# Kernel optimization log

Measured on AMD Instinct MI355X. Metric: run time of the kernel, lower is better.

## Reference

```python
import jax, jax.numpy as jnp
import numpy as np

B, S, D_IN, D_MID, D_OUT, V = 32, 512, 768, 128, 4, 100000
N = B * S  # static upper bound on number of unique (vocab_id, batch_id) pairs


def setup_inputs() -> dict:
    key = jax.random.key(0)
    k1, k2, k3, k4 = jax.random.split(key, 4)
    vocab_ids = jax.random.randint(k1, (B, S), 0, V)
    embeddings = jax.random.normal(k2, (B, S, D_IN), jnp.float32)
    # nn.Linear default init (kaiming-uniform-ish); exact distribution is irrelevant for correctness
    lin_bound = 1.0 / np.sqrt(D_IN)
    W1 = jax.random.uniform(k3, (D_IN, D_MID), jnp.float32, -lin_bound, lin_bound)
    b1 = jnp.zeros((D_MID,), jnp.float32)
    # kaiming_uniform_(a=sqrt(5)) on (V, D_MID, D_OUT): fan_in = D_MID*D_OUT, bound = 1/sqrt(fan_in)
    enc_bound = 1.0 / np.sqrt(D_MID * D_OUT)
    encoder_weights = jax.random.uniform(k4, (V, D_MID, D_OUT), jnp.float32, -enc_bound, enc_bound)
    return {"vocab_ids": vocab_ids, "embeddings": embeddings, "W1": W1, "b1": b1,
            "encoder_weights": encoder_weights}


def reference(vocab_ids, embeddings, W1, b1, encoder_weights):
    # Composite key = vocab_id * B + batch_id -> same lexicographic (vocab, batch) order
    # as torch.unique(dim=0) on stacked (vocab_id, batch_id) pairs.
    batch_ids = jnp.arange(B, dtype=vocab_ids.dtype)[:, None]            # (B,1)
    keys = (vocab_ids * B + batch_ids).reshape(-1)                        # (N,)
    # Static-size unique for jit; padded slots (fill) receive zero-sum embeddings.
    uniq_keys, inv = jnp.unique(keys, size=N, fill_value=0, return_inverse=True)
    flat_emb = embeddings.reshape(N, D_IN)
    summed = jax.ops.segment_sum(flat_emb, inv.reshape(-1), num_segments=N)  # (N, D_IN)
    h = jnp.tanh(summed @ W1 + b1)                                        # (N, D_MID)
    uniq_vocab = uniq_keys // B
    uniq_batch = uniq_keys % B
    Wtok = encoder_weights[uniq_vocab]                                    # (N, D_MID, D_OUT) gather
    encoded = jax.nn.sigmoid(jnp.einsum('bi,bio->bo', h, Wtok))           # (N, D_OUT)
    ids = jnp.stack([uniq_vocab, uniq_batch], axis=1)                     # (N, 2)
    return ids, encoded
```

## Files before the change

kernel.cpp:

```cpp
#include <hip/hip_runtime.h>
#include <hip/hip_bf16.h>

#define NELEM 16384
#define DIN 768
#define DMID 128
#define DOUT 4

typedef __attribute__((ext_vector_type(8))) short short8;
typedef __attribute__((ext_vector_type(4))) float f32x4;

__device__ __forceinline__ unsigned f2bf(float f) {
    unsigned u = __float_as_uint(f);
    return (u + 0x7FFFu + ((u >> 16) & 1u)) >> 16;
}
__device__ __forceinline__ unsigned wscan_inc(unsigned x, int lane) {
    unsigned inc = x;
#pragma unroll
    for (int off = 1; off < 64; off <<= 1) {
        unsigned y = __shfl_up(inc, off);
        if (lane >= off) inc += y;
    }
    return inc;
}

#define FAST6_WS 983168

__global__ __launch_bounds__(256) void prep_kernel(
    const int* __restrict__ vocab_ids, const float* __restrict__ W1,
    unsigned* __restrict__ Gb, unsigned short* __restrict__ WtG,
    unsigned* __restrict__ RB, unsigned long long* __restrict__ stage,
    unsigned* __restrict__ LCnt) {
    const int t = threadIdx.x;
    const int blk = blockIdx.x;

    if (blk >= 32) {
        int o = (blk - 32) * 1024 + t * 4;
        int c = o / DIN;
        int k = o - c * DIN;
        unsigned p0 = f2bf(W1[(k + 0) * DMID + c]) | (f2bf(W1[(k + 1) * DMID + c]) << 16);
        unsigned p1 = f2bf(W1[(k + 2) * DMID + c]) | (f2bf(W1[(k + 3) * DMID + c]) << 16);
        uint2 pk2; pk2.x = p0; pk2.y = p1;
        *(uint2*)(WtG + (size_t)c * DIN + k) = pk2;
        return;
    }

    __shared__ unsigned lbm[4096];
    __shared__ unsigned voc[512];
    __shared__ unsigned short gel[512];
    __shared__ unsigned gcnt[512];
    __shared__ unsigned gstart[512];
    __shared__ unsigned part[256];
    __shared__ unsigned wsumL[4];

    const int b = blk;
    const int lane = t & 63;
    const int wv = t >> 6;

#pragma unroll
    for (int i = 0; i < 16; ++i) lbm[t + 256 * i] = 0;
    gcnt[t] = 0; gcnt[t + 256] = 0;
#pragma unroll
    for (int q = 0; q < 2; ++q) {
        int s = q * 256 + t;
        voc[s] = (unsigned)vocab_ids[b * 512 + s];
    }
    __syncthreads();
#pragma unroll
    for (int q = 0; q < 2; ++q) {
        unsigned v = voc[q * 256 + t];
        atomicOr(&lbm[v >> 5], 1u << (v & 31u));
    }
    __syncthreads();
#pragma unroll
    for (int i = 0; i < 4; ++i) {
        int w4 = i * 256 + t;
        uint4 x;
        x.x = lbm[w4 * 4 + 0]; x.y = lbm[w4 * 4 + 1];
        x.z = lbm[w4 * 4 + 2]; x.w = lbm[w4 * 4 + 3];
        *(uint4*)(RB + (size_t)b * 4096 + w4 * 4) = x;
    }
    {
        unsigned sum = 0;
#pragma unroll
        for (int j = 0; j < 16; ++j) sum += (unsigned)__popc(lbm[t * 16 + j]);
        unsigned inc = wscan_inc(sum, lane);
        if (lane == 63) wsumL[wv] = inc;
        __syncthreads();
        unsigned woff = 0;
        for (int i = 0; i < wv; ++i) woff += wsumL[i];
        part[t] = woff + inc - sum;
        if (t == 255) LCnt[b] = woff + inc;
        __syncthreads();
    }
#pragma unroll
    for (int q = 0; q < 2; ++q) {
        int s = q * 256 + t;
        unsigned v = voc[s];
        unsigned lw = v >> 5, c = lw >> 4;
        unsigned g = part[c];
        for (unsigned j = c * 16; j < lw; ++j) g += (unsigned)__popc(lbm[j]);
        g += (unsigned)__popc(lbm[lw] & ((1u << (v & 31u)) - 1u));
        gel[s] = (unsigned short)g;
        atomicAdd(&gcnt[g], 1u);
    }
    __syncthreads();
    {
        unsigned a = gcnt[2 * t], b2 = gcnt[2 * t + 1];
        unsigned pair = a + b2;
        unsigned inc = wscan_inc(pair, lane);
        if (lane == 63) wsumL[wv] = inc;
        __syncthreads();
        unsigned woff = 0;
        for (int i = 0; i < wv; ++i) woff += wsumL[i];
        unsigned excl = woff + inc - pair;
        gstart[2 * t] = excl;
        gstart[2 * t + 1] = excl + a;
    }
    __syncthreads();
#pragma unroll
    for (int q = 0; q < 2; ++q) {
        int s = q * 256 + t;
        unsigned g = gel[s];
        unsigned v = voc[s];
        unsigned m = 0;
        if (gcnt[g] > 1) {
            for (int j = 0; j < s; ++j) if (voc[j] == v) ++m;
        }
        Gb[b * 512 + gstart[g] + m] = (v << 9) | (unsigned)s;
        if (m == 0) {
            unsigned sdval = ((unsigned)b << 19) | (gstart[g] << 10) | gcnt[g];
            stage[b * 512 + g] = ((unsigned long long)v << 32) | sdval;
        }
    }
}

__global__ __launch_bounds__(256) void rank_kernel(
    const unsigned* __restrict__ RB,
    const unsigned long long* __restrict__ stage,
    const unsigned* __restrict__ LCnt,
    unsigned* __restrict__ SD, float* __restrict__ out_ids) {
    __shared__ unsigned pre1[4096];
    __shared__ unsigned wsumL[4];
    __shared__ unsigned Ush;

    const int t = threadIdx.x;
    const int b = blockIdx.x;
    const int lane = t & 63;
    const int wv = t >> 6;
    const uint4* rb4 = (const uint4*)RB;

    {
        unsigned cs[16];
#pragma unroll
        for (int i = 0; i < 16; ++i) cs[i] = 0;
#pragma unroll 4
        for (int b2 = 0; b2 < 32; ++b2) {
            const uint4* rp = rb4 + b2 * 1024 + t * 4;
#pragma unroll
            for (int q = 0; q < 4; ++q) {
                uint4 x = rp[q];
                cs[q * 4 + 0] += (unsigned)__popc(x.x);
                cs[q * 4 + 1] += (unsigned)__popc(x.y);
                cs[q * 4 + 2] += (unsigned)__popc(x.z);
                cs[q * 4 + 3] += (unsigned)__popc(x.w);
            }
        }
        unsigned loc[16];
        unsigned run = 0;
#pragma unroll
        for (int i = 0; i < 16; ++i) { loc[i] = run; run += cs[i]; }
        unsigned inc = wscan_inc(run, lane);
        if (lane == 63) wsumL[wv] = inc;
        __syncthreads();
        unsigned woff = 0;
        for (int i = 0; i < wv; ++i) woff += wsumL[i];
        unsigned excl = woff + inc - run;
#pragma unroll
        for (int i = 0; i < 16; ++i) pre1[t * 16 + i] = excl + loc[i];
        if (t == 255) Ush = woff + inc;
        __syncthreads();
    }
    const unsigned U = Ush;

    const unsigned cnt = LCnt[b];
    for (unsigned l = t; l < cnt; l += 256) {
        unsigned long long sv = stage[b * 512 + l];
        unsigned v = (unsigned)(sv >> 32);
        unsigned sdval = (unsigned)sv;
        unsigned w = v >> 5, bit = v & 31u;
        unsigned maskLT = (1u << bit) - 1u;
        unsigned rank = pre1[w];
#pragma unroll 8
        for (int b2 = 0; b2 < 32; ++b2) {
            unsigned word = RB[b2 * 4096 + w];
            rank += (unsigned)__popc(word & maskLT);
            if (b2 < b) rank += (word >> bit) & 1u;
        }
        SD[rank] = sdval;
        out_ids[2 * rank + 0] = (float)v;
        out_ids[2 * rank + 1] = (float)b;
    }
    for (int u = (int)U + b * 256 + t; u < NELEM; u += 32 * 256) {
        SD[u] = 0u;
        out_ids[2 * u + 0] = 0.0f;
        out_ids[2 * u + 1] = 0.0f;
    }
}

#define FBM 16
__global__ __launch_bounds__(256) void fused_kernel(
    const unsigned* __restrict__ Gb,
    const unsigned* __restrict__ SD,
    const unsigned short* __restrict__ WtG,
    const float* __restrict__ emb,
    const float* __restrict__ b1,
    const float* __restrict__ enc,
    float* __restrict__ out_enc) {
    __shared__ char smem[20736];

    const int t = threadIdx.x;
    const int u0 = blockIdx.x * FBM;
    const int l = t & 63;
    const int w = t >> 6;

    const int ar = t >> 4;
    const int ak4 = t & 15;
    const unsigned sdw = SD[u0 + ar];
    const int lenA = (int)(sdw & 1023u);
    const unsigned embBase = (sdw >> 19) << 9;
    const unsigned gb0 = embBase + ((sdw >> 10) & 511u);

    f32x4 acc0 = {0.f, 0.f, 0.f, 0.f};
    f32x4 acc1 = {0.f, 0.f, 0.f, 0.f};

    for (int kk = 0; kk < DIN; kk += 64) {
        __syncthreads();
        {
            float s0 = 0.f, s1 = 0.f, s2 = 0.f, s3 = 0.f;
            const float* base = emb + (size_t)(kk + ak4 * 4);
            for (int p = 0; p < lenA; ++p) {
                unsigned idx = embBase + (Gb[gb0 + p] & 511u);
                const float4 e4 = *(const float4*)(base + (size_t)idx * DIN);
                s0 += e4.x; s1 += e4.y; s2 += e4.z; s3 += e4.w;
            }
            uint2 packed;
            packed.x = f2bf(s0) | (f2bf(s1) << 16);
            packed.y = f2bf(s2) | (f2bf(s3) << 16);
            *(uint2*)(smem + ar * 144 + ak4 * 8) = packed;
        }
        {
#pragma unroll
            for (int i = 0; i < 4; ++i) {
                int q = t + i * 256;
                int c = q >> 3;
                int uo = q & 7;
                uint4 dv = *(const uint4*)(WtG + (size_t)c * DIN + kk + uo * 8);
                *(uint4*)(smem + 2304 + c * 144 + uo * 16) = dv;
            }
        }
        __syncthreads();
        {
            const int arow = l & 15;
            const int ull = l >> 4;
#pragma unroll
            for (int kf = 0; kf < 2; ++kf) {
                short8 aF = *(const short8*)(smem + arow * 144 + kf * 64 + ull * 16);
                short8 bF0 = *(const short8*)(smem + 2304 + (w * 32 + arow) * 144 + kf * 64 + ull * 16);
                short8 bF1 = *(const short8*)(smem + 2304 + (w * 32 + 16 + arow) * 144 + kf * 64 + ull * 16);
                acc0 = __builtin_amdgcn_mfma_f32_16x16x32_bf16(aF, bF0, acc0, 0, 0, 0);
                acc1 = __builtin_amdgcn_mfma_f32_16x16x32_bf16(aF, bF1, acc1, 0, 0, 0);
            }
        }
    }
    __syncthreads();
    {
        float* Hs = (float*)smem;
        const int col0 = w * 32 + (l & 15);
        const int rbase = (l >> 4) * 4;
#pragma unroll
        for (int reg = 0; reg < 4; ++reg) {
            Hs[(rbase + reg) * 132 + col0] = tanhf(acc0[reg] + b1[col0]);
            Hs[(rbase + reg) * 132 + col0 + 16] = tanhf(acc1[reg] + b1[col0 + 16]);
        }
    }
    __syncthreads();
    {
        const float* Hs = (const float*)smem;
        const int r = t >> 4;
        const int g = t & 15;
        const int u = u0 + r;
        const unsigned sdw2 = SD[u];
        unsigned vocab = 0;
        if (sdw2 & 1023u)
            vocab = Gb[((sdw2 >> 19) << 9) + ((sdw2 >> 10) & 511u)] >> 9;
        const float4* wrow = (const float4*)(enc + (size_t)vocab * (DMID * DOUT));
        float ax = 0.f, ay = 0.f, az = 0.f, aw = 0.f;
#pragma unroll
        for (int jj = 0; jj < 8; ++jj) {
            int j = jj * 16 + g;
            float4 w4 = wrow[j];
            float hv = Hs[r * 132 + j];
            ax += hv * w4.x; ay += hv * w4.y; az += hv * w4.z; aw += hv * w4.w;
        }
#pragma unroll
        for (int off = 1; off < 16; off <<= 1) {
            ax += __shfl_xor(ax, off);
            ay += __shfl_xor(ay, off);
            az += __shfl_xor(az, off);
            aw += __shfl_xor(aw, off);
        }
        if (g == 0) {
            float4 o;
            o.x = 1.f / (1.f + expf(-ax));
            o.y = 1.f / (1.f + expf(-ay));
            o.z = 1.f / (1.f + expf(-az));
            o.w = 1.f / (1.f + expf(-aw));
            *(float4*)(out_enc + (size_t)u * 4) = o;
        }
    }
}

#define SORT_SMEM (65536 + 65536 + 4096 + 64)

__global__ __launch_bounds__(1024) void sort_transpose_kernel(
    const int* __restrict__ vocab_ids,
    const float* __restrict__ W1,
    unsigned int* __restrict__ G,
    unsigned short* __restrict__ RS,
    unsigned short* __restrict__ WtG,
    float* __restrict__ out_ids) {
    const int t = threadIdx.x;
    if (blockIdx.x != 0) {
        int idx = (blockIdx.x - 1) * 1024 + t;
        if (idx < DMID * DIN) {
            int c = idx / DIN;
            int k = idx - c * DIN;
            WtG[idx] = (unsigned short)f2bf(W1[k * DMID + c]);
        }
        return;
    }
    extern __shared__ char smem[];
    unsigned* Gs     = (unsigned*)smem;
    unsigned* histDM = (unsigned*)(smem + 65536);
    unsigned* sums   = (unsigned*)(smem + 131072);
    unsigned* totalU = (unsigned*)(smem + 135168);
    for (int e = t; e < NELEM; e += 1024)
        Gs[e] = ((unsigned)vocab_ids[e] << 14) | (unsigned)e;
    __syncthreads();
    for (int pass = 0; pass < 6; ++pass) {
        const int shift = 9 + pass * 4;
        unsigned v[16];
#pragma unroll
        for (int i = 0; i < 16; ++i) v[i] = Gs[t * 16 + i];
#pragma unroll
        for (int d = 0; d < 16; ++d) histDM[d * 1024 + t] = 0;
#pragma unroll
        for (int i = 0; i < 16; ++i) histDM[((v[i] >> shift) & 15u) * 1024 + t] += 1;
        __syncthreads();
        unsigned lex[16]; unsigned run = 0;
#pragma unroll
        for (int i = 0; i < 16; ++i) { unsigned x = histDM[t * 16 + i]; lex[i] = run; run += x; }
        sums[t] = run;
        __syncthreads();
        if (t < 64) {
            unsigned s[16]; unsigned tot = 0;
#pragma unroll
            for (int i = 0; i < 16; ++i) { unsigned x = sums[t * 16 + i]; s[i] = tot; tot += x; }
            unsigned incv = tot;
#pragma unroll
            for (int off = 1; off < 64; off <<= 1) {
                unsigned y = __shfl_up(incv, off);
                if (t >= off) incv += y;
            }
            unsigned excl = incv - tot;
#pragma unroll
            for (int i = 0; i < 16; ++i) sums[t * 16 + i] = excl + s[i];
        }
        __syncthreads();
#pragma unroll
        for (int i = 0; i < 16; ++i) histDM[t * 16 + i] = sums[t] + lex[i];
        __syncthreads();
        unsigned mycnt[16];
#pragma unroll
        for (int d = 0; d < 16; ++d) mycnt[d] = histDM[d * 1024 + t];
#pragma unroll
        for (int i = 0; i < 16; ++i) {
            unsigned d = (v[i] >> shift) & 15u;
            Gs[mycnt[d]++] = v[i];
        }
        __syncthreads();
    }
    unsigned v[16];
#pragma unroll
    for (int i = 0; i < 16; ++i) v[i] = Gs[t * 16 + i];
    unsigned pk = (t == 0) ? 0xFFFFFFFFu : (Gs[t * 16 - 1] >> 9);
    unsigned fm = 0;
#pragma unroll
    for (int i = 0; i < 16; ++i) {
        unsigned key = v[i] >> 9;
        if (key != pk) fm |= (1u << i);
        pk = key;
    }
    sums[t] = (unsigned)__popc(fm);
    __syncthreads();
    if (t < 64) {
        unsigned s[16]; unsigned tot = 0;
#pragma unroll
        for (int i = 0; i < 16; ++i) { unsigned x = sums[t * 16 + i]; s[i] = tot; tot += x; }
        unsigned incv = tot;
#pragma unroll
        for (int off = 1; off < 64; off <<= 1) {
            unsigned y = __shfl_up(incv, off);
            if (t >= off) incv += y;
        }
        unsigned excl = incv - tot;
#pragma unroll
        for (int i = 0; i < 16; ++i) sums[t * 16 + i] = excl + s[i];
        if (t == 63) *totalU = incv;
    }
    __syncthreads();
    unsigned r = sums[t];
#pragma unroll
    for (int i = 0; i < 16; ++i) {
        if (fm & (1u << i)) {
            RS[r] = (unsigned short)(t * 16 + i);
            out_ids[2 * r + 0] = (float)(v[i] >> 14);
            out_ids[2 * r + 1] = (float)((v[i] >> 9) & 31u);
            ++r;
        }
    }
    const unsigned U = *totalU;
    for (int u = t; u < NELEM; u += 1024) {
        if ((unsigned)u >= U) {
            RS[u] = (unsigned short)NELEM;
            out_ids[2 * u + 0] = 0.0f;
            out_ids[2 * u + 1] = 0.0f;
        }
        G[u] = Gs[u];
    }
    if (t == 0) RS[NELEM] = (unsigned short)NELEM;
}

__global__ __launch_bounds__(256) void fused_kernel_rs(
    const unsigned* __restrict__ G,
    const unsigned short* __restrict__ RS,
    const unsigned short* __restrict__ WtG,
    const float* __restrict__ emb,
    const float* __restrict__ b1,
    const float* __restrict__ enc,
    float* __restrict__ out_enc) {
    __shared__ char smem[20736];
    const int t = threadIdx.x;
    const int u0 = blockIdx.x * FBM;
    const int l = t & 63;
    const int w = t >> 6;
    const int ar = t >> 4;
    const int ak4 = t & 15;
    const int rs_a = (int)RS[u0 + ar];
    const int re_a = (int)RS[u0 + ar + 1];
    f32x4 acc0 = {0.f, 0.f, 0.f, 0.f};
    f32x4 acc1 = {0.f, 0.f, 0.f, 0.f};
    for (int kk = 0; kk < DIN; kk += 64) {
        __syncthreads();
        {
            float s0 = 0.f, s1 = 0.f, s2 = 0.f, s3 = 0.f;
            const float* base = emb + (size_t)(kk + ak4 * 4);
            for (int p = rs_a; p < re_a; ++p) {
                unsigned idx = G[p] & 16383u;
                const float4 e4 = *(const float4*)(base + (size_t)idx * DIN);
                s0 += e4.x; s1 += e4.y; s2 += e4.z; s3 += e4.w;
            }
            uint2 packed;
            packed.x = f2bf(s0) | (f2bf(s1) << 16);
            packed.y = f2bf(s2) | (f2bf(s3) << 16);
            *(uint2*)(smem + ar * 144 + ak4 * 8) = packed;
        }
        {
#pragma unroll
            for (int i = 0; i < 4; ++i) {
                int q = t + i * 256;
                int c = q >> 3;
                int uo = q & 7;
                uint4 dv = *(const uint4*)(WtG + (size_t)c * DIN + kk + uo * 8);
                *(uint4*)(smem + 2304 + c * 144 + uo * 16) = dv;
            }
        }
        __syncthreads();
        {
            const int arow = l & 15;
            const int ull = l >> 4;
#pragma unroll
            for (int kf = 0; kf < 2; ++kf) {
                short8 aF = *(const short8*)(smem + arow * 144 + kf * 64 + ull * 16);
                short8 bF0 = *(const short8*)(smem + 2304 + (w * 32 + arow) * 144 + kf * 64 + ull * 16);
                short8 bF1 = *(const short8*)(smem + 2304 + (w * 32 + 16 + arow) * 144 + kf * 64 + ull * 16);
                acc0 = __builtin_amdgcn_mfma_f32_16x16x32_bf16(aF, bF0, acc0, 0, 0, 0);
                acc1 = __builtin_amdgcn_mfma_f32_16x16x32_bf16(aF, bF1, acc1, 0, 0, 0);
            }
        }
    }
    __syncthreads();
    {
        float* Hs = (float*)smem;
        const int col0 = w * 32 + (l & 15);
        const int rbase = (l >> 4) * 4;
#pragma unroll
        for (int reg = 0; reg < 4; ++reg) {
            Hs[(rbase + reg) * 132 + col0] = tanhf(acc0[reg] + b1[col0]);
            Hs[(rbase + reg) * 132 + col0 + 16] = tanhf(acc1[reg] + b1[col0 + 16]);
        }
    }
    __syncthreads();
    {
        const float* Hs = (const float*)smem;
        const int r = t >> 4;
        const int g = t & 15;
        const int u = u0 + r;
        const int rs = (int)RS[u];
        const int re = (int)RS[u + 1];
        unsigned vocab = (rs < re) ? (G[rs] >> 14) : 0u;
        const float4* wrow = (const float4*)(enc + (size_t)vocab * (DMID * DOUT));
        float ax = 0.f, ay = 0.f, az = 0.f, aw = 0.f;
#pragma unroll
        for (int jj = 0; jj < 8; ++jj) {
            int j = jj * 16 + g;
            float4 w4 = wrow[j];
            float hv = Hs[r * 132 + j];
            ax += hv * w4.x; ay += hv * w4.y; az += hv * w4.z; aw += hv * w4.w;
        }
#pragma unroll
        for (int off = 1; off < 16; off <<= 1) {
            ax += __shfl_xor(ax, off);
            ay += __shfl_xor(ay, off);
            az += __shfl_xor(az, off);
            aw += __shfl_xor(aw, off);
        }
        if (g == 0) {
            float4 o;
            o.x = 1.f / (1.f + expf(-ax));
            o.y = 1.f / (1.f + expf(-ay));
            o.z = 1.f / (1.f + expf(-az));
            o.w = 1.f / (1.f + expf(-aw));
            *(float4*)(out_enc + (size_t)u * 4) = o;
        }
    }
}

extern "C" void kernel_launch(void* const* d_in, const int* in_sizes, int n_in,
                              void* d_out, int out_size, void* d_ws, size_t ws_size,
                              hipStream_t stream) {
    const int*   vocab_ids = (const int*)d_in[0];
    const float* emb       = (const float*)d_in[1];
    const float* W1        = (const float*)d_in[2];
    const float* b1        = (const float*)d_in[3];
    const float* enc       = (const float*)d_in[4];
    float* out = (float*)d_out;
    float* out_ids = out;
    float* out_enc = out + NELEM * 2;
    char* ws = (char*)d_ws;

    if (ws_size >= FAST6_WS) {
        unsigned*           Gb    = (unsigned*)(ws + 0);
        unsigned*           SD    = (unsigned*)(ws + 65536);
        unsigned short*     WtG   = (unsigned short*)(ws + 131072);
        unsigned long long* stage = (unsigned long long*)(ws + 327680);
        unsigned*           LCnt  = (unsigned*)(ws + 458752);
        unsigned*           RB    = (unsigned*)(ws + 458880);

        prep_kernel<<<128, 256, 0, stream>>>(vocab_ids, W1, Gb, WtG, RB, stage, LCnt);
        rank_kernel<<<32, 256, 0, stream>>>(RB, stage, LCnt, SD, out_ids);
        fused_kernel<<<NELEM / FBM, 256, 0, stream>>>(Gb, SD, WtG, emb, b1, enc, out_enc);
    } else {
        unsigned int*   G   = (unsigned int*)(ws);
        unsigned short* RS  = (unsigned short*)(ws + 65536);
        unsigned short* WtG = (unsigned short*)(ws + 98432);

        hipFuncSetAttribute((const void*)sort_transpose_kernel,
                            hipFuncAttributeMaxDynamicSharedMemorySize, SORT_SMEM);
        sort_transpose_kernel<<<1 + 96, 1024, SORT_SMEM, stream>>>(
            vocab_ids, W1, G, RS, WtG, out_ids);
        fused_kernel_rs<<<NELEM / FBM, 256, 0, stream>>>(G, RS, WtG, emb, b1, enc, out_enc);
    }
}
```

Before: 60.08 us.

## Merge prep and rank kernels into one launch with grid-wide atomic barriers

Combines the bitmap/group-building prep kernel and the rank kernel into a single 64-block kernel that uses atomic-counter grid barriers instead of a kernel boundary. The bf16 transpose of W1 is spread over 32 blocks instead of 96. The column popcount reduction over the 32 batch bitmaps is spread across all 64 blocks and stored in a small CS buffer, so the rank phase reads precomputed counts instead of each block re-reading the full bitmap set. Adds nontemporal stores and a memset for the barrier counter, and relies on all 64 blocks being co-resident.

```diff
diff --git a/kernel.cpp b/kernel.cpp
--- a/kernel.cpp
+++ b/kernel.cpp
@@ -8,6 +8,8 @@
 
 typedef __attribute__((ext_vector_type(8))) short short8;
 typedef __attribute__((ext_vector_type(4))) float f32x4;
+typedef __attribute__((ext_vector_type(2))) unsigned uint32x2;
+typedef __attribute__((ext_vector_type(4))) unsigned uint32x4;
 
 __device__ __forceinline__ unsigned f2bf(float f) {
     unsigned u = __float_as_uint(f);
@@ -23,147 +25,165 @@
     return inc;
 }
 
-#define FAST6_WS 983168
-
-__global__ __launch_bounds__(256) void prep_kernel(
+__device__ __forceinline__ void gbar(unsigned* cnt, unsigned thresh) {
+    __syncthreads();
+    if (threadIdx.x == 0) {
+        __hip_atomic_fetch_add(cnt, 1u, __ATOMIC_ACQ_REL, __HIP_MEMORY_SCOPE_AGENT);
+        while (__hip_atomic_load(cnt, __ATOMIC_RELAXED, __HIP_MEMORY_SCOPE_AGENT) < thresh)
+            __builtin_amdgcn_s_sleep(1);
+        (void)__hip_atomic_load(cnt, __ATOMIC_ACQUIRE, __HIP_MEMORY_SCOPE_AGENT);
+    }
+    __syncthreads();
+}
+
+#define FAST7_WS 999616
+
+__global__ __launch_bounds__(256) void merged_kernel(
     const int* __restrict__ vocab_ids, const float* __restrict__ W1,
-    unsigned* __restrict__ Gb, unsigned short* __restrict__ WtG,
-    unsigned* __restrict__ RB, unsigned long long* __restrict__ stage,
-    unsigned* __restrict__ LCnt) {
-    const int t = threadIdx.x;
-    const int blk = blockIdx.x;
-
-    if (blk >= 32) {
-        int o = (blk - 32) * 1024 + t * 4;
-        int c = o / DIN;
-        int k = o - c * DIN;
-        unsigned p0 = f2bf(W1[(k + 0) * DMID + c]) | (f2bf(W1[(k + 1) * DMID + c]) << 16);
-        unsigned p1 = f2bf(W1[(k + 2) * DMID + c]) | (f2bf(W1[(k + 3) * DMID + c]) << 16);
-        uint2 pk2; pk2.x = p0; pk2.y = p1;
-        *(uint2*)(WtG + (size_t)c * DIN + k) = pk2;
-        return;
-    }
-
+    unsigned* __restrict__ Gb, unsigned* __restrict__ SD,
+    unsigned short* __restrict__ WtG,
+    unsigned long long* __restrict__ stage, unsigned* __restrict__ LCnt,
+    unsigned* __restrict__ RB, unsigned* __restrict__ CS,
+    unsigned* __restrict__ bar, float* __restrict__ out_ids) {
     __shared__ unsigned lbm[4096];
     __shared__ unsigned voc[512];
     __shared__ unsigned short gel[512];
     __shared__ unsigned gcnt[512];
     __shared__ unsigned gstart[512];
     __shared__ unsigned part[256];
+    __shared__ unsigned colred[256];
     __shared__ unsigned wsumL[4];
-
-    const int b = blk;
+    __shared__ unsigned Ush;
+
+    const int t = threadIdx.x;
+    const int blk = blockIdx.x;
     const int lane = t & 63;
     const int wv = t >> 6;
 
-#pragma unroll
-    for (int i = 0; i < 16; ++i) lbm[t + 256 * i] = 0;
-    gcnt[t] = 0; gcnt[t + 256] = 0;
-#pragma unroll
-    for (int q = 0; q < 2; ++q) {
-        int s = q * 256 + t;
-        voc[s] = (unsigned)vocab_ids[b * 512 + s];
-    }
-    __syncthreads();
-#pragma unroll
-    for (int q = 0; q < 2; ++q) {
-        unsigned v = voc[q * 256 + t];
-        atomicOr(&lbm[v >> 5], 1u << (v & 31u));
-    }
-    __syncthreads();
-#pragma unroll
-    for (int i = 0; i < 4; ++i) {
-        int w4 = i * 256 + t;
-        uint4 x;
-        x.x = lbm[w4 * 4 + 0]; x.y = lbm[w4 * 4 + 1];
-        x.z = lbm[w4 * 4 + 2]; x.w = lbm[w4 * 4 + 3];
-        *(uint4*)(RB + (size_t)b * 4096 + w4 * 4) = x;
-    }
+    if (blk >= 32) {
+        int base = (blk - 32) * 256 + t;
+        int c = base >> 6;
+        int k0 = (base & 63) * 12;
+#pragma unroll
+        for (int j = 0; j < 3; ++j) {
+            int k = k0 + j * 4;
+            uint32x2 pk2;
+            pk2.x = f2bf(W1[(k + 0) * DMID + c]) | (f2bf(W1[(k + 1) * DMID + c]) << 16);
+            pk2.y = f2bf(W1[(k + 2) * DMID + c]) | (f2bf(W1[(k + 3) * DMID + c]) << 16);
+            __builtin_nontemporal_store(pk2, (uint32x2*)(WtG + (size_t)c * DIN + k));
+        }
+    } else {
+        const int b = blk;
+#pragma unroll
+        for (int i = 0; i < 16; ++i) lbm[t + 256 * i] = 0;
+        gcnt[t] = 0; gcnt[t + 256] = 0;
+#pragma unroll
+        for (int q = 0; q < 2; ++q) {
+            int s = q * 256 + t;
+            voc[s] = (unsigned)vocab_ids[b * 512 + s];
+        }
+        __syncthreads();
+#pragma unroll
+        for (int q = 0; q < 2; ++q) {
+            unsigned v = voc[q * 256 + t];
+            atomicOr(&lbm[v >> 5], 1u << (v & 31u));
+        }
+        __syncthreads();
+#pragma unroll
+        for (int i = 0; i < 4; ++i) {
+            int w4 = i * 256 + t;
+            uint32x4 x;
+            x.x = lbm[w4 * 4 + 0]; x.y = lbm[w4 * 4 + 1];
+            x.z = lbm[w4 * 4 + 2]; x.w = lbm[w4 * 4 + 3];
+            __builtin_nontemporal_store(x, (uint32x4*)(RB + (size_t)b * 4096 + w4 * 4));
+        }
+        {
+            unsigned sum = 0;
+#pragma unroll
+            for (int j = 0; j < 16; ++j) sum += (unsigned)__popc(lbm[t * 16 + j]);
+            unsigned inc = wscan_inc(sum, lane);
+            if (lane == 63) wsumL[wv] = inc;
+            __syncthreads();
+            unsigned woff = 0;
+            for (int i = 0; i < wv; ++i) woff += wsumL[i];
+            part[t] = woff + inc - sum;
+            if (t == 255) __builtin_nontemporal_store(woff + inc, LCnt + b);
+            __syncthreads();
+        }
+#pragma unroll
+        for (int q = 0; q < 2; ++q) {
+            int s = q * 256 + t;
+            unsigned v = voc[s];
+            unsigned lw = v >> 5, c = lw >> 4;
+            unsigned g = part[c];
+            for (unsigned j = c * 16; j < lw; ++j) g += (unsigned)__popc(lbm[j]);
+            g += (unsigned)__popc(lbm[lw] & ((1u << (v & 31u)) - 1u));
+            gel[s] = (unsigned short)g;
+            atomicAdd(&gcnt[g], 1u);
+        }
+        __syncthreads();
+        {
+            unsigned a = gcnt[2 * t], b2 = gcnt[2 * t + 1];
+            unsigned pair = a + b2;
+            unsigned inc = wscan_inc(pair, lane);
+            if (lane == 63) wsumL[wv] = inc;
+            __syncthreads();
+            unsigned woff = 0;
+            for (int i = 0; i < wv; ++i) woff += wsumL[i];
+            unsigned excl = woff + inc - pair;
+            gstart[2 * t] = excl;
+            gstart[2 * t + 1] = excl + a;
+        }
+        __syncthreads();
+#pragma unroll
+        for (int q = 0; q < 2; ++q) {
+            int s = q * 256 + t;
+            unsigned g = gel[s];
+            unsigned v = voc[s];
+            unsigned m = 0;
+            if (gcnt[g] > 1) {
+                for (int j = 0; j < s; ++j) if (voc[j] == v) ++m;
+            }
+            __builtin_nontemporal_store((v << 9) | (unsigned)s,
+                                        Gb + b * 512 + gstart[g] + m);
+            if (m == 0) {
+                unsigned sdval = ((unsigned)b << 19) | (gstart[g] << 10) | gcnt[g];
+                __builtin_nontemporal_store(((unsigned long long)v << 32) | sdval,
+                                            stage + b * 512 + g);
+            }
+        }
+    }
+
+    gbar(bar, 64);
+
     {
-        unsigned sum = 0;
-#pragma unroll
-        for (int j = 0; j < 16; ++j) sum += (unsigned)__popc(lbm[t * 16 + j]);
-        unsigned inc = wscan_inc(sum, lane);
-        if (lane == 63) wsumL[wv] = inc;
-        __syncthreads();
-        unsigned woff = 0;
-        for (int i = 0; i < wv; ++i) woff += wsumL[i];
-        part[t] = woff + inc - sum;
-        if (t == 255) LCnt[b] = woff + inc;
-        __syncthreads();
-    }
-#pragma unroll
-    for (int q = 0; q < 2; ++q) {
-        int s = q * 256 + t;
-        unsigned v = voc[s];
-        unsigned lw = v >> 5, c = lw >> 4;
-        unsigned g = part[c];
-        for (unsigned j = c * 16; j < lw; ++j) g += (unsigned)__popc(lbm[j]);
-        g += (unsigned)__popc(lbm[lw] & ((1u << (v & 31u)) - 1u));
-        gel[s] = (unsigned short)g;
-        atomicAdd(&gcnt[g], 1u);
-    }
-    __syncthreads();
-    {
-        unsigned a = gcnt[2 * t], b2 = gcnt[2 * t + 1];
-        unsigned pair = a + b2;
-        unsigned inc = wscan_inc(pair, lane);
-        if (lane == 63) wsumL[wv] = inc;
-        __syncthreads();
-        unsigned woff = 0;
-        for (int i = 0; i < wv; ++i) woff += wsumL[i];
-        unsigned excl = woff + inc - pair;
-        gstart[2 * t] = excl;
-        gstart[2 * t + 1] = excl + a;
-    }
-    __syncthreads();
-#pragma unroll
-    for (int q = 0; q < 2; ++q) {
-        int s = q * 256 + t;
-        unsigned g = gel[s];
-        unsigned v = voc[s];
-        unsigned m = 0;
-        if (gcnt[g] > 1) {
-            for (int j = 0; j < s; ++j) if (voc[j] == v) ++m;
-        }
-        Gb[b * 512 + gstart[g] + m] = (v << 9) | (unsigned)s;
-        if (m == 0) {
-            unsigned sdval = ((unsigned)b << 19) | (gstart[g] << 10) | gcnt[g];
-            stage[b * 512 + g] = ((unsigned long long)v << 32) | sdval;
-        }
-    }
-}
-
-__global__ __launch_bounds__(256) void rank_kernel(
-    const unsigned* __restrict__ RB,
-    const unsigned long long* __restrict__ stage,
-    const unsigned* __restrict__ LCnt,
-    unsigned* __restrict__ SD, float* __restrict__ out_ids) {
-    __shared__ unsigned pre1[4096];
-    __shared__ unsigned wsumL[4];
-    __shared__ unsigned Ush;
-
-    const int t = threadIdx.x;
-    const int b = blockIdx.x;
-    const int lane = t & 63;
-    const int wv = t >> 6;
-    const uint4* rb4 = (const uint4*)RB;
-
+        const int w = blk * 64 + lane;
+        const int r0 = wv * 8;
+        unsigned partial = 0;
+#pragma unroll
+        for (int r = 0; r < 8; ++r)
+            partial += (unsigned)__popc(RB[(size_t)(r0 + r) * 4096 + w]);
+        colred[t] = partial;
+        __syncthreads();
+        if (t < 64) {
+            unsigned cs = colred[t] + colred[t + 64] + colred[t + 128] + colred[t + 192];
+            __builtin_nontemporal_store(cs, CS + blk * 64 + t);
+        }
+    }
+
+    gbar(bar, 128);
+
+    if (blk >= 32) return;
+
+    const int b = blk;
     {
         unsigned cs[16];
-#pragma unroll
-        for (int i = 0; i < 16; ++i) cs[i] = 0;
-#pragma unroll 4
-        for (int b2 = 0; b2 < 32; ++b2) {
-            const uint4* rp = rb4 + b2 * 1024 + t * 4;
-#pragma unroll
-            for (int q = 0; q < 4; ++q) {
-                uint4 x = rp[q];
-                cs[q * 4 + 0] += (unsigned)__popc(x.x);
-                cs[q * 4 + 1] += (unsigned)__popc(x.y);
-                cs[q * 4 + 2] += (unsigned)__popc(x.z);
-                cs[q * 4 + 3] += (unsigned)__popc(x.w);
-            }
+        const uint32x4* my = (const uint32x4*)CS + t * 4;
+#pragma unroll
+        for (int q = 0; q < 4; ++q) {
+            uint32x4 x = my[q];
+            cs[q * 4 + 0] = x.x; cs[q * 4 + 1] = x.y;
+            cs[q * 4 + 2] = x.z; cs[q * 4 + 3] = x.w;
         }
         unsigned loc[16];
         unsigned run = 0;
@@ -176,12 +196,11 @@
         for (int i = 0; i < wv; ++i) woff += wsumL[i];
         unsigned excl = woff + inc - run;
 #pragma unroll
-        for (int i = 0; i < 16; ++i) pre1[t * 16 + i] = excl + loc[i];
+        for (int i = 0; i < 16; ++i) lbm[t * 16 + i] = excl + loc[i];
         if (t == 255) Ush = woff + inc;
         __syncthreads();
     }
     const unsigned U = Ush;
-
     const unsigned cnt = LCnt[b];
     for (unsigned l = t; l < cnt; l += 256) {
         unsigned long long sv = stage[b * 512 + l];
@@ -189,19 +208,19 @@
         unsigned sdval = (unsigned)sv;
         unsigned w = v >> 5, bit = v & 31u;
         unsigned maskLT = (1u << bit) - 1u;
-        unsigned rank = pre1[w];
+        unsigned rank = lbm[w];
 #pragma unroll 8
         for (int b2 = 0; b2 < 32; ++b2) {
-            unsigned word = RB[b2 * 4096 + w];
+            unsigned word = RB[(size_t)b2 * 4096 + w];
             rank += (unsigned)__popc(word & maskLT);
             if (b2 < b) rank += (word >> bit) & 1u;
         }
-        SD[rank] = sdval;
+        __builtin_nontemporal_store(sdval, SD + rank);
         out_ids[2 * rank + 0] = (float)v;
         out_ids[2 * rank + 1] = (float)b;
     }
     for (int u = (int)U + b * 256 + t; u < NELEM; u += 32 * 256) {
-        SD[u] = 0u;
+        __builtin_nontemporal_store(0u, SD + u);
         out_ids[2 * u + 0] = 0.0f;
         out_ids[2 * u + 1] = 0.0f;
     }
@@ -559,24 +578,27 @@
     float* out_enc = out + NELEM * 2;
     char* ws = (char*)d_ws;
 
-    if (ws_size >= FAST6_WS) {
+    if (ws_size >= FAST7_WS) {
         unsigned*           Gb    = (unsigned*)(ws + 0);
         unsigned*           SD    = (unsigned*)(ws + 65536);
         unsigned short*     WtG   = (unsigned short*)(ws + 131072);
         unsigned long long* stage = (unsigned long long*)(ws + 327680);
         unsigned*           LCnt  = (unsigned*)(ws + 458752);
         unsigned*           RB    = (unsigned*)(ws + 458880);
-
-        prep_kernel<<<128, 256, 0, stream>>>(vocab_ids, W1, Gb, WtG, RB, stage, LCnt);
-        rank_kernel<<<32, 256, 0, stream>>>(RB, stage, LCnt, SD, out_ids);
+        unsigned*           CS    = (unsigned*)(ws + 983168);
+        unsigned*           bar   = (unsigned*)(ws + 999552);
+
+        (void)hipMemsetAsync(bar, 0, 4, stream);
+        merged_kernel<<<64, 256, 0, stream>>>(vocab_ids, W1, Gb, SD, WtG,
+                                              stage, LCnt, RB, CS, bar, out_ids);
         fused_kernel<<<NELEM / FBM, 256, 0, stream>>>(Gb, SD, WtG, emb, b1, enc, out_enc);
     } else {
         unsigned int*   G   = (unsigned int*)(ws);
         unsigned short* RS  = (unsigned short*)(ws + 65536);
         unsigned short* WtG = (unsigned short*)(ws + 98432);
 
-        hipFuncSetAttribute((const void*)sort_transpose_kernel,
-                            hipFuncAttributeMaxDynamicSharedMemorySize, SORT_SMEM);
+        (void)hipFuncSetAttribute((const void*)sort_transpose_kernel,
+                                  hipFuncAttributeMaxDynamicSharedMemorySize, SORT_SMEM);
         sort_transpose_kernel<<<1 + 96, 1024, SORT_SMEM, stream>>>(
             vocab_ids, W1, G, RS, WtG, out_ids);
         fused_kernel_rs<<<NELEM / FBM, 256, 0, stream>>>(G, RS, WtG, emb, b1, enc, out_enc);
```

After: 63.59 us. 5.8% more time.
